# Performance work log

Measured on AMD Instinct MI355X. Metric: run time of the kernel, lower is better.

Reference implementation:

```python
import jax, jax.numpy as jnp
import numpy as np

D_MODEL = 256
D_HID = 128
EPS = 1e-5
MASK_VALUE = -10000.0


def _layer_norm(x, scale, bias):
    mu = jnp.mean(x, axis=-1, keepdims=True)
    var = jnp.mean(jnp.square(x - mu), axis=-1, keepdims=True)
    return (x - mu) * jax.lax.rsqrt(var + EPS) * scale + bias


def setup_inputs() -> dict:
    key = jax.random.key(0)
    ks = jax.random.split(key, 8)
    B, S = 32, 1024
    std = 0.02
    return {
        "x": jax.random.normal(ks[0], (B, S, D_MODEL), dtype=jnp.float32),
        "ln1_scale": jnp.ones((D_MODEL,), jnp.float32),
        "ln1_bias": jnp.zeros((D_MODEL,), jnp.float32),
        "w_qkv": jax.random.normal(ks[1], (D_MODEL, 3 * D_MODEL), jnp.float32) * std,
        "b_qkv": jnp.zeros((3 * D_MODEL,), jnp.float32),
        "w_proj": jax.random.normal(ks[2], (D_MODEL, D_MODEL), jnp.float32) * std,
        "b_proj": jnp.zeros((D_MODEL,), jnp.float32),
        "ln2_scale": jnp.ones((D_MODEL,), jnp.float32),
        "ln2_bias": jnp.zeros((D_MODEL,), jnp.float32),
        "w_fc1": jax.random.normal(ks[3], (D_MODEL, D_HID), jnp.float32) * std,
        "b_fc1": jnp.zeros((D_HID,), jnp.float32),
        "w_fc2": jax.random.normal(ks[4], (D_HID, D_MODEL), jnp.float32) * std,
        "b_fc2": jnp.zeros((D_MODEL,), jnp.float32),
    }


def reference(x, ln1_scale, ln1_bias, w_qkv, b_qkv, w_proj, b_proj,
              ln2_scale, ln2_bias, w_fc1, b_fc1, w_fc2, b_fc2):
    B, S, D = x.shape
    # --- pre-LN self-attention ---
    residual = x
    h = _layer_norm(x, ln1_scale, ln1_bias)
    qkv = h @ w_qkv + b_qkv                       # [B, S, 3D]
    q, k, v = jnp.split(qkv, 3, axis=2)           # each [B, S, D]; 1 head, head_dim=D
    scale = 1.0 / jnp.sqrt(jnp.asarray(D, x.dtype))
    scores = jnp.einsum('bqd,bkd->bqk', q, k) * scale   # [B, S, S]
    causal = jnp.tril(jnp.ones((S, S), dtype=bool))
    scores = jnp.where(causal[None, :, :], scores, MASK_VALUE)
    attn = jax.nn.softmax(scores, axis=-1)        # dropout is identity (eval mode)
    out = jnp.einsum('bqk,bkd->bqd', attn, v)     # [B, S, D]
    out = out @ w_proj + b_proj
    x = out + residual
    # --- pre-LN MLP ---
    residual = x
    h = _layer_norm(x, ln2_scale, ln2_bias)
    h = jax.nn.relu(h @ w_fc1 + b_fc1)
    h = h @ w_fc2 + b_fc2
    return h + residual
```

## Files before the change

kernel.cpp:

```cpp
#include <hip/hip_runtime.h>
#include <hip/hip_bf16.h>

#define D_MODEL 256
#define D_HID   128
#define SEQ     1024
#define NBATCH  32
#define NROWS   (NBATCH * SEQ)
#define MASKV   -10000.0f
#define EPSLN   1e-5f

typedef unsigned short u16;
using bf16x8 = __attribute__((ext_vector_type(8))) short;
using f32x4  = __attribute__((ext_vector_type(4))) float;

union U8 { uint4 v; u16 s[8]; };

__device__ __forceinline__ float bf2f(u16 u) {
    unsigned int x = ((unsigned int)u) << 16;
    return __uint_as_float(x);
}
__device__ __forceinline__ u16 f2bf(float f) {
    unsigned int u = __float_as_uint(f);
    u += 0x7fff + ((u >> 16) & 1);
    return (u16)(u >> 16);
}
__device__ __forceinline__ void load4(const float* p, float* f) {
    float4 a = *(const float4*)p;
    f[0] = a.x; f[1] = a.y; f[2] = a.z; f[3] = a.w;
}
__device__ __forceinline__ void load4(const u16* p, float* f) {
    ushort4 v = *(const ushort4*)p;
    f[0] = bf2f(v.x); f[1] = bf2f(v.y); f[2] = bf2f(v.z); f[3] = bf2f(v.w);
}
__device__ __forceinline__ void gload16(const u16* g, u16* l) {
    __builtin_amdgcn_global_load_lds(
        (const __attribute__((address_space(1))) void*)g,
        (__attribute__((address_space(3))) void*)l, 16, 0, 0);
}

__global__ __launch_bounds__(256) void transpose_weights(
    const float* __restrict__ wqkv, u16* __restrict__ wqkvT,
    const float* __restrict__ wproj, u16* __restrict__ wprojT,
    const float* __restrict__ wfc1, u16* __restrict__ wfc1T,
    const float* __restrict__ wfc2, u16* __restrict__ wfc2T) {
    int tid = blockIdx.x * 256 + threadIdx.x;
    int stride = gridDim.x * 256;
    for (int i = tid; i < 768 * 256; i += stride) {
        int n = i >> 8, k = i & 255;
        wqkvT[i] = f2bf(wqkv[k * 768 + n]);
    }
    for (int i = tid; i < 256 * 256; i += stride) {
        int n = i >> 8, k = i & 255;
        wprojT[i] = f2bf(wproj[k * 256 + n]);
    }
    for (int i = tid; i < 128 * 256; i += stride) {
        int n = i >> 8, k = i & 255;
        wfc1T[i] = f2bf(wfc1[k * 128 + n]);
    }
    for (int i = tid; i < 256 * 128; i += stride) {
        int n = i >> 7, k = i & 127;
        wfc2T[i] = f2bf(wfc2[k * 256 + n]);
    }
}

template <typename TX>
__global__ __launch_bounds__(256) void ln_fused(
    const TX* __restrict__ x, const float* __restrict__ gamma,
    const float* __restrict__ beta, u16* __restrict__ out) {
    int wave = threadIdx.x >> 6, lane = threadIdx.x & 63;
    int row = blockIdx.x * 4 + wave;
    float f[4];
    load4(x + (size_t)row * D_MODEL + lane * 4, f);
    float s  = f[0] + f[1] + f[2] + f[3];
    float sq = f[0] * f[0] + f[1] * f[1] + f[2] * f[2] + f[3] * f[3];
    #pragma unroll
    for (int off = 1; off < 64; off <<= 1) {
        s  += __shfl_xor(s, off);
        sq += __shfl_xor(sq, off);
    }
    float mu   = s * (1.0f / 256.0f);
    float var  = sq * (1.0f / 256.0f) - mu * mu;
    float rstd = rsqrtf(var + EPSLN);
    float g[4], be[4];
    load4(gamma + lane * 4, g);
    load4(beta + lane * 4, be);
    ushort4 o;
    o.x = f2bf((f[0] - mu) * rstd * g[0] + be[0]);
    o.y = f2bf((f[1] - mu) * rstd * g[1] + be[1]);
    o.z = f2bf((f[2] - mu) * rstd * g[2] + be[2]);
    o.w = f2bf((f[3] - mu) * rstd * g[3] + be[3]);
    *(ushort4*)(out + (size_t)row * D_MODEL + lane * 4) = o;
}

#define GEMM_LDS_ELEMS ((128 + 64) * 136)

template <int K>
__device__ __forceinline__ void gemm_tile(
    const u16* __restrict__ A, const u16* __restrict__ BT,
    int m0, int n0, u16* lds, f32x4 acc[4][2]) {
    constexpr int KC = 128, KP = 136;
    u16* ldsA = lds;
    u16* ldsB = lds + 128 * KP;
    const int tid = threadIdx.x;
    const int lane = tid & 63, wave = tid >> 6;
    const int wr = (wave >> 1) * 64, wc = (wave & 1) * 32;
    const int row = lane & 15, quad = lane >> 4;

    for (int ks = 0; ks < K; ks += KC) {
        __syncthreads();
        for (int i = tid; i < 2048; i += 256) {
            int i8 = i * 8;
            int r = i8 >> 7, c = i8 & 127;
            *(uint4*)(ldsA + r * KP + c) =
                *(const uint4*)(A + (size_t)(m0 + r) * K + ks + c);
        }
        for (int i = tid; i < 1024; i += 256) {
            int i8 = i * 8;
            int r = i8 >> 7, c = i8 & 127;
            *(uint4*)(ldsB + r * KP + c) =
                *(const uint4*)(BT + (size_t)(n0 + r) * K + ks + c);
        }
        __syncthreads();
        #pragma unroll
        for (int k0 = 0; k0 < KC; k0 += 32) {
            bf16x8 a[4], b[2];
            #pragma unroll
            for (int mi = 0; mi < 4; mi++)
                a[mi] = *(const bf16x8*)(ldsA + (wr + mi * 16 + row) * KP + k0 + quad * 8);
            #pragma unroll
            for (int nj = 0; nj < 2; nj++)
                b[nj] = *(const bf16x8*)(ldsB + (wc + nj * 16 + row) * KP + k0 + quad * 8);
            #pragma unroll
            for (int mi = 0; mi < 4; mi++)
                #pragma unroll
                for (int nj = 0; nj < 2; nj++)
                    acc[mi][nj] = __builtin_amdgcn_mfma_f32_16x16x32_bf16(
                        a[mi], b[nj], acc[mi][nj], 0, 0, 0);
        }
    }
}

#define ZERO_ACC(acc)                                        \
    _Pragma("unroll") for (int i_ = 0; i_ < 4; i_++)         \
    _Pragma("unroll") for (int j_ = 0; j_ < 2; j_++)         \
    _Pragma("unroll") for (int e_ = 0; e_ < 4; e_++) acc[i_][j_][e_] = 0.0f;

#define EPILOG_IDX                                           \
    int lane = threadIdx.x & 63, wave = threadIdx.x >> 6;    \
    int wr = (wave >> 1) * 64, wc = (wave & 1) * 32;         \
    int row = lane & 15, quad = lane >> 4;

__global__ __launch_bounds__(256) void gemm_qkv(
    const u16* __restrict__ h, const u16* __restrict__ wqkvT,
    const float* __restrict__ b_qkv,
    u16* __restrict__ q, u16* __restrict__ kk, u16* __restrict__ vT) {
    __shared__ u16 lds[GEMM_LDS_ELEMS];
    f32x4 acc[4][2];
    ZERO_ACC(acc)
    int m0 = blockIdx.x * 128, n0 = blockIdx.y * 64;
    gemm_tile<256>(h, wqkvT, m0, n0, lds, acc);
    EPILOG_IDX
    #pragma unroll
    for (int mi = 0; mi < 4; mi++) {
        #pragma unroll
        for (int nj = 0; nj < 2; nj++) {
            int gn = n0 + wc + nj * 16 + row;
            float bias = b_qkv[gn];
            int gm = m0 + wr + mi * 16 + quad * 4;
            if (gn < 256) {
                #pragma unroll
                for (int r = 0; r < 4; r++)
                    q[(size_t)(gm + r) * 256 + gn] =
                        f2bf((acc[mi][nj][r] + bias) * 0.0625f);
            } else if (gn < 512) {
                int col = gn - 256;
                #pragma unroll
                for (int r = 0; r < 4; r++)
                    kk[(size_t)(gm + r) * 256 + col] = f2bf(acc[mi][nj][r] + bias);
            } else {
                int d = gn - 512;
                int b = gm >> 10, s = gm & 1023;
                ushort4 pack;
                pack.x = f2bf(acc[mi][nj][0] + bias);
                pack.y = f2bf(acc[mi][nj][1] + bias);
                pack.z = f2bf(acc[mi][nj][2] + bias);
                pack.w = f2bf(acc[mi][nj][3] + bias);
                *(ushort4*)(vT + ((size_t)(b * 256 + d) << 10) + s) = pack;
            }
        }
    }
}

__global__ __launch_bounds__(256) void gemm_proj(
    const u16* __restrict__ ao, const u16* __restrict__ wprojT,
    const float* __restrict__ b_proj, const float* __restrict__ x_in,
    u16* __restrict__ x2) {
    __shared__ u16 lds[GEMM_LDS_ELEMS];
    f32x4 acc[4][2];
    ZERO_ACC(acc)
    int m0 = blockIdx.x * 128, n0 = blockIdx.y * 64;
    gemm_tile<256>(ao, wprojT, m0, n0, lds, acc);
    EPILOG_IDX
    #pragma unroll
    for (int mi = 0; mi < 4; mi++)
        #pragma unroll
        for (int nj = 0; nj < 2; nj++) {
            int gn = n0 + wc + nj * 16 + row;
            float bias = b_proj[gn];
            int gm = m0 + wr + mi * 16 + quad * 4;
            #pragma unroll
            for (int r = 0; r < 4; r++) {
                size_t idx = (size_t)(gm + r) * 256 + gn;
                x2[idx] = f2bf(acc[mi][nj][r] + bias + x_in[idx]);
            }
        }
}

__global__ __launch_bounds__(256) void gemm_fc1(
    const u16* __restrict__ h2, const u16* __restrict__ wfc1T,
    const float* __restrict__ b_fc1, u16* __restrict__ a1) {
    __shared__ u16 lds[GEMM_LDS_ELEMS];
    f32x4 acc[4][2];
    ZERO_ACC(acc)
    int m0 = blockIdx.x * 128, n0 = blockIdx.y * 64;
    gemm_tile<256>(h2, wfc1T, m0, n0, lds, acc);
    EPILOG_IDX
    #pragma unroll
    for (int mi = 0; mi < 4; mi++)
        #pragma unroll
        for (int nj = 0; nj < 2; nj++) {
            int gn = n0 + wc + nj * 16 + row;
            float bias = b_fc1[gn];
            int gm = m0 + wr + mi * 16 + quad * 4;
            #pragma unroll
            for (int r = 0; r < 4; r++) {
                float v = acc[mi][nj][r] + bias;
                a1[(size_t)(gm + r) * 128 + gn] = f2bf(fmaxf(v, 0.0f));
            }
        }
}

__global__ __launch_bounds__(256) void gemm_fc2(
    const u16* __restrict__ a1, const u16* __restrict__ wfc2T,
    const float* __restrict__ b_fc2, const u16* __restrict__ x2,
    float* __restrict__ out) {
    __shared__ u16 lds[GEMM_LDS_ELEMS];
    f32x4 acc[4][2];
    ZERO_ACC(acc)
    int m0 = blockIdx.x * 128, n0 = blockIdx.y * 64;
    gemm_tile<128>(a1, wfc2T, m0, n0, lds, acc);
    EPILOG_IDX
    #pragma unroll
    for (int mi = 0; mi < 4; mi++)
        #pragma unroll
        for (int nj = 0; nj < 2; nj++) {
            int gn = n0 + wc + nj * 16 + row;
            float bias = b_fc2[gn];
            int gm = m0 + wr + mi * 16 + quad * 4;
            #pragma unroll
            for (int r = 0; r < 4; r++) {
                size_t idx = (size_t)(gm + r) * 256 + gn;
                out[idx] = acc[mi][nj][r] + bias + bf2f(x2[idx]);
            }
        }
}

__global__ __launch_bounds__(256) void attn_kernel(
    const u16* __restrict__ q, const u16* __restrict__ k,
    const u16* __restrict__ vT, u16* __restrict__ ao) {
    __shared__ u16 k_lds[2][32 * 256];
    __shared__ u16 v_lds[2][256 * 32];
    __shared__ u16 p_lds[4][16 * 40];

    int j = blockIdx.x;
    int b = j & 31, rr = j >> 5;
    int qt = (rr < 8) ? rr : 23 - rr;
    int tid = threadIdx.x;
    int lane = tid & 63, wave = tid >> 6;
    int row = lane & 15, quad = lane >> 4;
    int q0 = qt * 64;
    int qrow0 = q0 + wave * 16;

    const u16* qb = q + ((size_t)b << 10) * 256;
    const u16* kb = k + ((size_t)b << 10) * 256;
    const u16* vb = vT + (((size_t)b * 256) << 10);

    const int kxor = (row & 7) << 3;
    const int vxor = (row & 6) << 2;

    bf16x8 qf[8];
    #pragma unroll
    for (int kf = 0; kf < 8; kf++)
        qf[kf] = *(const bf16x8*)(qb + (size_t)(qrow0 + row) * 256 + kf * 32 + quad * 8);

    f32x4 o[16];
    #pragma unroll
    for (int n = 0; n < 16; n++)
        #pragma unroll
        for (int e = 0; e < 4; e++) o[n][e] = 0.0f;
    float m_i[4], l_i[4];
    #pragma unroll
    for (int r = 0; r < 4; r++) { m_i[r] = -1e30f; l_i[r] = 0.0f; }

    int nkt = 2 * qt + 2;
    int wlast = 2 * qt + (wave >> 1);

    auto stage = [&](int bf, int kt) {
        int k0 = kt << 5;
        #pragma unroll
        for (int c = 0; c < 4; c++) {
            int blk = wave * 4 + c;
            int B = (blk << 10) + lane * 16;
            int rk = B >> 9;
            int ck = (B & 511) ^ ((rk & 7) << 4);
            gload16(kb + (size_t)(k0 + rk) * 256 + (ck >> 1),
                    &k_lds[bf][blk << 9]);
            int rv = B >> 6;
            int cv = (B & 63) ^ ((rv & 6) << 3);
            gload16(vb + ((size_t)rv << 10) + k0 + (cv >> 1),
                    &v_lds[bf][blk << 9]);
        }
    };

    stage(0, 0);
    __syncthreads();

    for (int kt = 0; kt < nkt; kt++) {
        int cur = kt & 1;
        if (kt + 1 < nkt) stage(cur ^ 1, kt + 1);
        if (kt <= wlast) {
            const u16* kl = k_lds[cur];
            const u16* vl = v_lds[cur];

            f32x4 sf[2];
            #pragma unroll
            for (int jn = 0; jn < 2; jn++)
                #pragma unroll
                for (int e = 0; e < 4; e++) sf[jn][e] = 0.0f;
            __builtin_amdgcn_s_setprio(1);
            #pragma unroll
            for (int kf = 0; kf < 8; kf++)
                #pragma unroll
                for (int jn = 0; jn < 2; jn++) {
                    bf16x8 bfrag = *(const bf16x8*)(kl +
                        ((((jn * 16 + row) * 256) + kf * 32 + quad * 8) ^ kxor));
                    sf[jn] = __builtin_amdgcn_mfma_f32_16x16x32_bf16(
                        qf[kf], bfrag, sf[jn], 0, 0, 0);
                }
            __builtin_amdgcn_s_setprio(0);

            int kk0 = kt * 32;
            bool diag = (kt == wlast);
            int qrow = qrow0 + quad * 4;
            float sv[2][4];
            #pragma unroll
            for (int jn = 0; jn < 2; jn++)
                #pragma unroll
                for (int r = 0; r < 4; r++) {
                    float v = sf[jn][r];
                    if (diag && (kk0 + jn * 16 + row > qrow + r)) v = MASKV;
                    sv[jn][r] = v;
                }

            float pmax[4];
            int need = 0;
            #pragma unroll
            for (int r = 0; r < 4; r++) {
                float t = fmaxf(sv[0][r], sv[1][r]);
                t = fmaxf(t, __shfl_xor(t, 1));
                t = fmaxf(t, __shfl_xor(t, 2));
                t = fmaxf(t, __shfl_xor(t, 4));
                t = fmaxf(t, __shfl_xor(t, 8));
                pmax[r] = t;
                need |= (t > m_i[r] + 8.0f) ? 1 : 0;
            }
            if (__any(need)) {
                #pragma unroll
                for (int r = 0; r < 4; r++) {
                    float mnew = fmaxf(m_i[r], pmax[r]);
                    float al = __expf(m_i[r] - mnew);
                    m_i[r] = mnew;
                    l_i[r] *= al;
                    #pragma unroll
                    for (int n = 0; n < 16; n++) o[n][r] *= al;
                }
            }
            #pragma unroll
            for (int r = 0; r < 4; r++) {
                float ps = 0.0f;
                #pragma unroll
                for (int jn = 0; jn < 2; jn++) {
                    sv[jn][r] = __expf(sv[jn][r] - m_i[r]);
                    ps += sv[jn][r];
                }
                ps += __shfl_xor(ps, 1);
                ps += __shfl_xor(ps, 2);
                ps += __shfl_xor(ps, 4);
                ps += __shfl_xor(ps, 8);
                l_i[r] += ps;
            }

            u16* pw = p_lds[wave];
            #pragma unroll
            for (int jn = 0; jn < 2; jn++)
                #pragma unroll
                for (int r = 0; r < 4; r++)
                    pw[(quad * 4 + r) * 40 + jn * 16 + row] = f2bf(sv[jn][r]);
            bf16x8 pf = *(const bf16x8*)(pw + row * 40 + quad * 8);

            __builtin_amdgcn_s_setprio(1);
            #pragma unroll
            for (int n = 0; n < 16; n++) {
                bf16x8 bv = *(const bf16x8*)(vl +
                    ((((n * 16 + row) * 32) + quad * 8) ^ vxor));
                o[n] = __builtin_amdgcn_mfma_f32_16x16x32_bf16(pf, bv, o[n], 0, 0, 0);
            }
            __builtin_amdgcn_s_setprio(0);
        }
        __syncthreads();
    }

    float inv[4];
    #pragma unroll
    for (int r = 0; r < 4; r++) inv[r] = 1.0f / l_i[r];
    u16* aob = ao + (((size_t)b << 10) + qrow0) * 256;
    #pragma unroll
    for (int r = 0; r < 4; r++)
        #pragma unroll
        for (int n = 0; n < 16; n++)
            aob[(size_t)(quad * 4 + r) * 256 + n * 16 + row] =
                f2bf(o[n][r] * inv[r]);
}

extern "C" void kernel_launch(void* const* d_in, const int* in_sizes, int n_in,
                              void* d_out, int out_size, void* d_ws, size_t ws_size,
                              hipStream_t stream) {
    const float* x      = (const float*)d_in[0];
    const float* ln1_s  = (const float*)d_in[1];
    const float* ln1_b  = (const float*)d_in[2];
    const float* w_qkv  = (const float*)d_in[3];
    const float* b_qkv  = (const float*)d_in[4];
    const float* w_proj = (const float*)d_in[5];
    const float* b_proj = (const float*)d_in[6];
    const float* ln2_s  = (const float*)d_in[7];
    const float* ln2_b  = (const float*)d_in[8];
    const float* w_fc1  = (const float*)d_in[9];
    const float* b_fc1  = (const float*)d_in[10];
    const float* w_fc2  = (const float*)d_in[11];
    const float* b_fc2  = (const float*)d_in[12];
    float* out = (float*)d_out;

    u16* h  = (u16*)d_out;
    u16* h2 = h + (size_t)NROWS * 256;

    u16* W = (u16*)d_ws;
    u16* wqkvT  = W;
    u16* wprojT = wqkvT + 196608;
    u16* wfc1T  = wprojT + 65536;
    u16* wfc2T  = wfc1T + 32768;
    u16* buf1   = wfc2T + 32768;
    u16* buf2   = buf1 + (size_t)NROWS * 256;
    u16* buf3   = buf2 + (size_t)NROWS * 256;

    transpose_weights<<<dim3(64), dim3(256), 0, stream>>>(
        w_qkv, wqkvT, w_proj, wprojT, w_fc1, wfc1T, w_fc2, wfc2T);
    ln_fused<float><<<dim3(NROWS / 4), dim3(256), 0, stream>>>(
        x, ln1_s, ln1_b, h);
    gemm_qkv<<<dim3(NROWS / 128, 12), dim3(256), 0, stream>>>(
        h, wqkvT, b_qkv, buf1, buf2, buf3);
    attn_kernel<<<dim3(512), dim3(256), 0, stream>>>(
        buf1, buf2, buf3, buf1);
    gemm_proj<<<dim3(NROWS / 128, 4), dim3(256), 0, stream>>>(
        buf1, wprojT, b_proj, x, buf2);
    ln_fused<u16><<<dim3(NROWS / 4), dim3(256), 0, stream>>>(
        buf2, ln2_s, ln2_b, h2);
    gemm_fc1<<<dim3(NROWS / 128, 2), dim3(256), 0, stream>>>(
        h2, wfc1T, b_fc1, buf3);
    gemm_fc2<<<dim3(NROWS / 128, 4), dim3(256), 0, stream>>>(
        buf3, wfc2T, b_fc2, buf2, out);
}
```

Baseline: 278.1 us.

## Split long causal attention tiles across two blocks and merge partials

The attention kernel now splits the KV range of the eight longest query tiles per batch (qt 8..15) into two halves, each handled by its own block. Each half writes an unnormalized bf16 partial output plus per-row max and sum, and a new attn_merge kernel combines them with log-sum-exp rescaling. This balances work across 768 blocks instead of 512 so the longest blocks no longer set the tail. The cost is an extra launch, a partial-buffer round trip, and an extra bf16 rounding of the partials. Row reductions also switch from shfl_xor to DPP moves.

```diff
diff --git a/kernel.cpp b/kernel.cpp
--- a/kernel.cpp
+++ b/kernel.cpp
@@ -36,6 +36,26 @@
     __builtin_amdgcn_global_load_lds(
         (const __attribute__((address_space(1))) void*)g,
         (__attribute__((address_space(3))) void*)l, 16, 0, 0);
+}
+
+template <int CTRL>
+__device__ __forceinline__ float dpp_mov(float v) {
+    return __int_as_float(__builtin_amdgcn_update_dpp(
+        0, __float_as_int(v), CTRL, 0xf, 0xf, true));
+}
+__device__ __forceinline__ float red16_max(float v) {
+    v = fmaxf(v, dpp_mov<0xB1>(v));
+    v = fmaxf(v, dpp_mov<0x4E>(v));
+    v = fmaxf(v, dpp_mov<0x141>(v));
+    v = fmaxf(v, dpp_mov<0x140>(v));
+    return v;
+}
+__device__ __forceinline__ float red16_sum(float v) {
+    v += dpp_mov<0xB1>(v);
+    v += dpp_mov<0x4E>(v);
+    v += dpp_mov<0x141>(v);
+    v += dpp_mov<0x140>(v);
+    return v;
 }
 
 __global__ __launch_bounds__(256) void transpose_weights(
@@ -265,16 +285,26 @@
         }
 }
 
+__constant__ unsigned char WQT[24] = {7,15,15,14,14,6,13,13,12,12,5,11,
+                                      11,10,10,4,9,9,8,8,3,2,1,0};
+__constant__ unsigned char WH[24]  = {2,0,1,0,1,2,0,1,0,1,2,0,
+                                      1,0,1,2,0,1,0,1,2,2,2,2};
+
 __global__ __launch_bounds__(256) void attn_kernel(
     const u16* __restrict__ q, const u16* __restrict__ k,
-    const u16* __restrict__ vT, u16* __restrict__ ao) {
+    const u16* __restrict__ vT, u16* __restrict__ ao,
+    u16* __restrict__ part, float* __restrict__ ml) {
     __shared__ u16 k_lds[2][32 * 256];
     __shared__ u16 v_lds[2][256 * 32];
     __shared__ u16 p_lds[4][16 * 40];
 
     int j = blockIdx.x;
-    int b = j & 31, rr = j >> 5;
-    int qt = (rr < 8) ? rr : 23 - rr;
+    int b = j & 31, w = j >> 5;
+    int qt = WQT[w], hh = WH[w];
+    int lo, hi;
+    if (hh == 2) { lo = 0; hi = 2 * qt + 2; }
+    else         { lo = hh * (qt + 1); hi = lo + qt + 1; }
+
     int tid = threadIdx.x;
     int lane = tid & 63, wave = tid >> 6;
     int row = lane & 15, quad = lane >> 4;
@@ -302,7 +332,6 @@
     #pragma unroll
     for (int r = 0; r < 4; r++) { m_i[r] = -1e30f; l_i[r] = 0.0f; }
 
-    int nkt = 2 * qt + 2;
     int wlast = 2 * qt + (wave >> 1);
 
     auto stage = [&](int bf, int kt) {
@@ -322,12 +351,12 @@
         }
     };
 
-    stage(0, 0);
+    stage(0, lo);
     __syncthreads();
 
-    for (int kt = 0; kt < nkt; kt++) {
-        int cur = kt & 1;
-        if (kt + 1 < nkt) stage(cur ^ 1, kt + 1);
+    for (int kt = lo; kt < hi; kt++) {
+        int cur = (kt - lo) & 1;
+        if (kt + 1 < hi) stage(cur ^ 1, kt + 1);
         if (kt <= wlast) {
             const u16* kl = k_lds[cur];
             const u16* vl = v_lds[cur];
@@ -366,13 +395,8 @@
             int need = 0;
             #pragma unroll
             for (int r = 0; r < 4; r++) {
-                float t = fmaxf(sv[0][r], sv[1][r]);
-                t = fmaxf(t, __shfl_xor(t, 1));
-                t = fmaxf(t, __shfl_xor(t, 2));
-                t = fmaxf(t, __shfl_xor(t, 4));
-                t = fmaxf(t, __shfl_xor(t, 8));
-                pmax[r] = t;
-                need |= (t > m_i[r] + 8.0f) ? 1 : 0;
+                pmax[r] = red16_max(fmaxf(sv[0][r], sv[1][r]));
+                need |= (pmax[r] > m_i[r] + 8.0f) ? 1 : 0;
             }
             if (__any(need)) {
                 #pragma unroll
@@ -393,11 +417,7 @@
                     sv[jn][r] = __expf(sv[jn][r] - m_i[r]);
                     ps += sv[jn][r];
                 }
-                ps += __shfl_xor(ps, 1);
-                ps += __shfl_xor(ps, 2);
-                ps += __shfl_xor(ps, 4);
-                ps += __shfl_xor(ps, 8);
-                l_i[r] += ps;
+                l_i[r] += red16_sum(ps);
             }
 
             u16* pw = p_lds[wave];
@@ -420,16 +440,67 @@
         __syncthreads();
     }
 
-    float inv[4];
-    #pragma unroll
-    for (int r = 0; r < 4; r++) inv[r] = 1.0f / l_i[r];
-    u16* aob = ao + (((size_t)b << 10) + qrow0) * 256;
-    #pragma unroll
-    for (int r = 0; r < 4; r++)
-        #pragma unroll
-        for (int n = 0; n < 16; n++)
-            aob[(size_t)(quad * 4 + r) * 256 + n * 16 + row] =
-                f2bf(o[n][r] * inv[r]);
+    if (hh == 2) {
+        float inv[4];
+        #pragma unroll
+        for (int r = 0; r < 4; r++) inv[r] = 1.0f / l_i[r];
+        u16* aob = ao + (((size_t)b << 10) + qrow0) * 256;
+        #pragma unroll
+        for (int r = 0; r < 4; r++)
+            #pragma unroll
+            for (int n = 0; n < 16; n++)
+                aob[(size_t)(quad * 4 + r) * 256 + n * 16 + row] =
+                    f2bf(o[n][r] * inv[r]);
+    } else {
+        int p = (((b << 3) | (qt - 8)) << 1) | hh;
+        u16* pb = part + (((size_t)p) << 6) * 256;
+        #pragma unroll
+        for (int r = 0; r < 4; r++) {
+            int rt = wave * 16 + quad * 4 + r;
+            #pragma unroll
+            for (int n = 0; n < 16; n++)
+                pb[(size_t)rt * 256 + n * 16 + row] = f2bf(o[n][r]);
+        }
+        if (row == 0) {
+            #pragma unroll
+            for (int r = 0; r < 4; r++) {
+                int rt = wave * 16 + quad * 4 + r;
+                float2 v2; v2.x = m_i[r]; v2.y = l_i[r];
+                *(float2*)(ml + ((size_t)((p << 6) + rt)) * 2) = v2;
+            }
+        }
+    }
+}
+
+__global__ __launch_bounds__(256) void attn_merge(
+    const u16* __restrict__ part, const float* __restrict__ ml,
+    u16* __restrict__ ao) {
+    int j = blockIdx.x;
+    int b = j >> 3, qi = j & 7;
+    int t = threadIdx.x;
+    int r = t >> 2, cq = t & 3;
+    int pA = j << 1, pB = pA | 1;
+    const float* mlA = ml + ((size_t)(pA << 6) + r) * 2;
+    const float* mlB = ml + ((size_t)(pB << 6) + r) * 2;
+    float mA = mlA[0], lA = mlA[1];
+    float mB = mlB[0], lB = mlB[1];
+    float m  = fmaxf(mA, mB);
+    float eA = __expf(mA - m), eB = __expf(mB - m);
+    float inv = 1.0f / (lA * eA + lB * eB);
+    float sA = eA * inv, sB = eB * inv;
+    const u16* oA = part + (((size_t)(pA << 6) + r) * 256) + cq * 64;
+    const u16* oB = part + (((size_t)(pB << 6) + r) * 256) + cq * 64;
+    u16* dst = ao + ((size_t)((b << 10) + 512 + (qi << 6) + r)) * 256 + cq * 64;
+    #pragma unroll
+    for (int u = 0; u < 8; u++) {
+        U8 a, bb, o;
+        a.v  = *(const uint4*)(oA + u * 8);
+        bb.v = *(const uint4*)(oB + u * 8);
+        #pragma unroll
+        for (int e = 0; e < 8; e++)
+            o.s[e] = f2bf(bf2f(a.s[e]) * sA + bf2f(bb.s[e]) * sB);
+        *(uint4*)(dst + u * 8) = o.v;
+    }
 }
 
 extern "C" void kernel_launch(void* const* d_in, const int* in_sizes, int n_in,
@@ -462,14 +533,19 @@
     u16* buf2   = buf1 + (size_t)NROWS * 256;
     u16* buf3   = buf2 + (size_t)NROWS * 256;
 
+    u16*   part  = h;
+    float* mlbuf = (float*)h2;
+
     transpose_weights<<<dim3(64), dim3(256), 0, stream>>>(
         w_qkv, wqkvT, w_proj, wprojT, w_fc1, wfc1T, w_fc2, wfc2T);
     ln_fused<float><<<dim3(NROWS / 4), dim3(256), 0, stream>>>(
         x, ln1_s, ln1_b, h);
     gemm_qkv<<<dim3(NROWS / 128, 12), dim3(256), 0, stream>>>(
         h, wqkvT, b_qkv, buf1, buf2, buf3);
-    attn_kernel<<<dim3(512), dim3(256), 0, stream>>>(
-        buf1, buf2, buf3, buf1);
+    attn_kernel<<<dim3(768), dim3(256), 0, stream>>>(
+        buf1, buf2, buf3, buf1, part, mlbuf);
+    attn_merge<<<dim3(256), dim3(256), 0, stream>>>(
+        part, mlbuf, buf1);
     gemm_proj<<<dim3(NROWS / 128, 4), dim3(256), 0, stream>>>(
         buf1, wprojT, b_proj, x, buf2);
     ln_fused<u16><<<dim3(NROWS / 4), dim3(256), 0, stream>>>(
```

Result: no change. 274.9 us (-1.2%).
